# Performance work log

Measured on AMD Instinct MI355X. Metric: run time of the kernel, lower is better.

The kernel has to match this reference:

```python
import jax, jax.numpy as jnp
import numpy as np

N = 50000        # nodes
E = 800000       # random edges (self loops appended inside reference, per PyG default)
IN = 128         # in_channels
H1, C1 = 8, 64   # conv1: heads, hidden_channels
NUM_CLASSES = 2  # conv2 out (heads=1, concat=False)
NEG_SLOPE = 0.2  # PyG GATConv default LeakyReLU slope


def setup_inputs() -> dict:
    key = jax.random.key(0)
    ks = jax.random.split(key, 12)
    x = jax.random.normal(ks[0], (N, IN), dtype=jnp.float32)
    edge_index = jax.random.randint(ks[1], (2, E), 0, N)
    # conv1 params: W1 [IN, H1*C1], att vectors [H1, C1], bias [H1*C1]
    W1 = jax.random.normal(ks[2], (IN, H1 * C1), dtype=jnp.float32) / np.sqrt(IN)
    a_src1 = jax.random.normal(ks[3], (H1, C1), dtype=jnp.float32) / np.sqrt(C1)
    a_dst1 = jax.random.normal(ks[4], (H1, C1), dtype=jnp.float32) / np.sqrt(C1)
    b1 = jnp.zeros((H1 * C1,), dtype=jnp.float32)
    # conv2 params: heads=1, out=NUM_CLASSES
    W2 = jax.random.normal(ks[5], (H1 * C1, 1 * NUM_CLASSES), dtype=jnp.float32) / np.sqrt(H1 * C1)
    a_src2 = jax.random.normal(ks[6], (1, NUM_CLASSES), dtype=jnp.float32) / np.sqrt(NUM_CLASSES)
    a_dst2 = jax.random.normal(ks[7], (1, NUM_CLASSES), dtype=jnp.float32) / np.sqrt(NUM_CLASSES)
    b2 = jnp.zeros((NUM_CLASSES,), dtype=jnp.float32)
    return {"x": x, "edge_index": edge_index, "W1": W1, "a_src1": a_src1,
            "a_dst1": a_dst1, "b1": b1, "W2": W2, "a_src2": a_src2,
            "a_dst2": a_dst2, "b2": b2}


def gat_layer(x, src, dst, W, a_src, a_dst, bias, concat):
    n = x.shape[0]
    heads, ch = a_src.shape
    h = (x @ W).reshape(n, heads, ch)                      # [N,H,C]
    alpha_s = jnp.einsum('nhc,hc->nh', h, a_src)           # per-node src score
    alpha_d = jnp.einsum('nhc,hc->nh', h, a_dst)           # per-node dst score
    e = jax.nn.leaky_relu(alpha_s[src] + alpha_d[dst], NEG_SLOPE)  # [Etot,H]
    # segment softmax over edges grouped by destination node
    m = jax.ops.segment_max(e, dst, num_segments=n)
    ex = jnp.exp(e - m[dst])
    den = jax.ops.segment_sum(ex, dst, num_segments=n)
    alpha = ex / den[dst]                                  # [Etot,H]
    out = jax.ops.segment_sum(h[src] * alpha[:, :, None], dst, num_segments=n)  # [N,H,C]
    out = out.reshape(n, heads * ch) if concat else out.mean(axis=1)
    return out + bias


def reference(x, edge_index, W1, a_src1, a_dst1, b1, W2, a_src2, a_dst2, b2):
    n = x.shape[0]
    loops = jnp.arange(n, dtype=edge_index.dtype)
    src = jnp.concatenate([edge_index[0], loops])   # PyG add_self_loops=True
    dst = jnp.concatenate([edge_index[1], loops])
    h = gat_layer(x, src, dst, W1, a_src1, a_dst1, b1, concat=True)   # [N, H1*C1]
    h = jax.nn.elu(h)
    # dropout is identity in eval mode
    out = gat_layer(h, src, dst, W2, a_src2, a_dst2, b2, concat=False)  # [N, 2]
    return out
```

## Files before the change

kernel.cpp:

```cpp
#include <hip/hip_runtime.h>
#include <hip/hip_bf16.h>

#define NEG 0.2f
#define BKT 64

typedef __attribute__((ext_vector_type(8))) short bf16x8;
typedef __attribute__((ext_vector_type(4))) float f32x4;
typedef __attribute__((ext_vector_type(4))) unsigned int u32x4;

static __device__ __forceinline__ unsigned short f2bf(float f) {
    union { float f; unsigned u; } v; v.f = f;
    unsigned r = v.u + 0x7fff + ((v.u >> 16) & 1);
    return (unsigned short)(r >> 16);
}
static __device__ __forceinline__ float bf_lo(unsigned u) {
    return __uint_as_float(u << 16);
}
static __device__ __forceinline__ float bf_hi(unsigned u) {
    return __uint_as_float(u & 0xffff0000u);
}

__global__ void k_init(int* __restrict__ deg, unsigned short* __restrict__ csr, int n) {
    int v = blockIdx.x * 256 + threadIdx.x;
    if (v >= n) return;
    deg[v] = 1;
    csr[(size_t)v * BKT] = (unsigned short)v;
}

__global__ __launch_bounds__(256) void k_big(const int* __restrict__ ei,
                                             int* __restrict__ deg,
                                             unsigned short* __restrict__ csr,
                                             const float* __restrict__ x,
                                             const float* __restrict__ W1,
                                             const float* __restrict__ a_src,
                                             const float* __restrict__ a_dst,
                                             unsigned short* __restrict__ h1b,
                                             float* __restrict__ as1,
                                             float* __restrict__ ad1,
                                             int E_, int n, int gblocks) {
    int tid = threadIdx.x;
    if ((int)blockIdx.x >= gblocks) {
        int e = (blockIdx.x - gblocks) * 256 + tid;
        if (e >= E_) return;
        int s = ei[e], d = ei[E_ + e];
        int slot = atomicAdd(&deg[d], 1);
        if (slot < BKT) csr[(size_t)d * BKT + slot] = (unsigned short)s;
        return;
    }
    __shared__ unsigned short stg[4][16][72];
    int wave = tid >> 6, lane = tid & 63;
    int l15 = lane & 15, q = lane >> 4;
    int rowblk = blockIdx.x * 256 + wave * 64;

    bf16x8 xf[4][4];
    #pragma unroll
    for (int st = 0; st < 4; st++) {
        int ar = rowblk + st * 16 + l15; if (ar > n - 1) ar = n - 1;
        const float* ap = x + (size_t)ar * 128 + q * 8;
        #pragma unroll
        for (int kb = 0; kb < 4; kb++) {
            float4 v0 = *(const float4*)(ap + kb * 32);
            float4 v1 = *(const float4*)(ap + kb * 32 + 4);
            xf[st][kb][0] = (short)f2bf(v0.x); xf[st][kb][1] = (short)f2bf(v0.y);
            xf[st][kb][2] = (short)f2bf(v0.z); xf[st][kb][3] = (short)f2bf(v0.w);
            xf[st][kb][4] = (short)f2bf(v1.x); xf[st][kb][5] = (short)f2bf(v1.y);
            xf[st][kb][6] = (short)f2bf(v1.z); xf[st][kb][7] = (short)f2bf(v1.w);
        }
    }

    for (int j = 0; j < 8; j++) {
        int col0 = j * 64;
        bf16x8 bfr[4][4];
        #pragma unroll
        for (int kb = 0; kb < 4; kb++)
            #pragma unroll
            for (int t = 0; t < 4; t++) {
                const float* wp = W1 + (size_t)(kb * 32 + q * 8) * 512 + col0 + t * 16 + l15;
                #pragma unroll
                for (int e = 0; e < 8; e++)
                    bfr[kb][t][e] = (short)f2bf(wp[(size_t)e * 512]);
            }
        float asv[4], adv[4];
        #pragma unroll
        for (int t = 0; t < 4; t++) {
            asv[t] = a_src[j * 64 + t * 16 + l15];
            adv[t] = a_dst[j * 64 + t * 16 + l15];
        }

        #pragma unroll
        for (int st = 0; st < 4; st++) {
            int row0 = rowblk + st * 16;
            f32x4 acc[4] = {};
            #pragma unroll
            for (int kb = 0; kb < 4; kb++)
                #pragma unroll
                for (int t = 0; t < 4; t++)
                    acc[t] = __builtin_amdgcn_mfma_f32_16x16x32_bf16(xf[st][kb], bfr[kb][t], acc[t], 0, 0, 0);
            #pragma unroll
            for (int t = 0; t < 4; t++)
                #pragma unroll
                for (int r = 0; r < 4; r++)
                    stg[wave][q * 4 + r][t * 16 + l15] = f2bf(acc[t][r]);
            #pragma unroll
            for (int p = 0; p < 2; p++) {
                int lr = p * 8 + (lane >> 3);
                int row = row0 + lr;
                int cd = (lane & 7) * 8;
                uint4 vv = *(const uint4*)&stg[wave][lr][cd];
                int slice = 2 * j + (cd >> 5);
                if (row < n)
                    *(uint4*)(h1b + ((size_t)slice * n + row) * 32 + (cd & 31)) = vv;
            }
            float ps[4], pd[4];
            #pragma unroll
            for (int r = 0; r < 4; r++) {
                ps[r] = acc[0][r] * asv[0] + acc[1][r] * asv[1]
                      + acc[2][r] * asv[2] + acc[3][r] * asv[3];
                pd[r] = acc[0][r] * adv[0] + acc[1][r] * adv[1]
                      + acc[2][r] * adv[2] + acc[3][r] * adv[3];
                #pragma unroll
                for (int off = 1; off < 16; off <<= 1) {
                    ps[r] += __shfl_xor(ps[r], off, 64);
                    pd[r] += __shfl_xor(pd[r], off, 64);
                }
            }
            if (l15 < 4) {
                int r = l15;
                float vps = ps[0], vpd = pd[0];
                if (r == 1) { vps = ps[1]; vpd = pd[1]; }
                if (r == 2) { vps = ps[2]; vpd = pd[2]; }
                if (r == 3) { vps = ps[3]; vpd = pd[3]; }
                int row = row0 + q * 4 + r;
                if (row < n) {
                    as1[(size_t)j * n + row] = vps;
                    ad1[(size_t)j * n + row] = vpd;
                }
            }
        }
    }
}

#define ACC1(Wt_, Hv_) \
    acc[0] = fmaf(Wt_, bf_lo(Hv_.x), acc[0]); \
    acc[1] = fmaf(Wt_, bf_hi(Hv_.x), acc[1]); \
    acc[2] = fmaf(Wt_, bf_lo(Hv_.y), acc[2]); \
    acc[3] = fmaf(Wt_, bf_hi(Hv_.y), acc[3]); \
    acc[4] = fmaf(Wt_, bf_lo(Hv_.z), acc[4]); \
    acc[5] = fmaf(Wt_, bf_hi(Hv_.z), acc[5]); \
    acc[6] = fmaf(Wt_, bf_lo(Hv_.w), acc[6]); \
    acc[7] = fmaf(Wt_, bf_hi(Hv_.w), acc[7]);

__global__ __launch_bounds__(256) void k_agg1(const unsigned short* __restrict__ h1b,
                                              const float* __restrict__ as1,
                                              const float* __restrict__ ad1,
                                              const float* __restrict__ b1,
                                              const float* __restrict__ W2,
                                              const int* __restrict__ deg,
                                              const unsigned short* __restrict__ csr,
                                              float* __restrict__ part,
                                              int n, int bpp) {
    int b = blockIdx.x;
    int xcd = b & 7;
    int t = b >> 3;
    int sp = (t >= bpp) ? 1 : 0;
    int j = t - sp * bpp;
    int slice = xcd + 8 * sp;
    int head = slice >> 1;

    __shared__ unsigned short idx[4][16][72];

    int tid = threadIdx.x;
    int lane = tid & 63, wave = tid >> 6;
    int g = lane >> 2, sub = lane & 3;
    int v = j * 64 + wave * 16 + g;
    bool act = v < n;
    int vc = act ? v : (n - 1);

    const u32x4* cb = (const u32x4*)(csr + (size_t)vc * BKT);
    u32x4 c0 = __builtin_nontemporal_load(cb + sub);
    u32x4 c1 = __builtin_nontemporal_load(cb + 4 + sub);
    *(u32x4*)&idx[wave][g][sub * 8] = c0;
    *(u32x4*)&idx[wave][g][32 + sub * 8] = c1;
    __syncthreads();

    const unsigned short* hs = h1b + (size_t)slice * n * 32 + sub * 8;
    const float* as1h = as1 + (size_t)head * n;
    const unsigned short* ip = &idx[wave][g][0];

    float adh = 0.f;
    int dv = 0;
    if (act) {
        adh = ad1[(size_t)head * n + v];
        dv = deg[v];
        if (dv > BKT) dv = BKT;
    }

    float s = 0.f;
    float acc[8] = {};
    int i = 0;
    for (; i + 8 <= dv; i += 8) {
        ushort4 ua = *(const ushort4*)(ip + i);
        ushort4 ub = *(const ushort4*)(ip + i + 4);
        int u0 = ua.x, u1 = ua.y, u2 = ua.z, u3 = ua.w;
        int u4 = ub.x, u5 = ub.y, u6 = ub.z, u7 = ub.w;
        float e0 = as1h[u0], e1 = as1h[u1], e2 = as1h[u2], e3 = as1h[u3];
        float e4 = as1h[u4], e5 = as1h[u5], e6 = as1h[u6], e7 = as1h[u7];
        uint4 h0 = *(const uint4*)(hs + (size_t)u0 * 32);
        uint4 h1 = *(const uint4*)(hs + (size_t)u1 * 32);
        uint4 h2 = *(const uint4*)(hs + (size_t)u2 * 32);
        uint4 h3 = *(const uint4*)(hs + (size_t)u3 * 32);
        uint4 h4 = *(const uint4*)(hs + (size_t)u4 * 32);
        uint4 h5 = *(const uint4*)(hs + (size_t)u5 * 32);
        uint4 h6 = *(const uint4*)(hs + (size_t)u6 * 32);
        uint4 h7 = *(const uint4*)(hs + (size_t)u7 * 32);
        e0 += adh; e1 += adh; e2 += adh; e3 += adh;
        e4 += adh; e5 += adh; e6 += adh; e7 += adh;
        e0 = (e0 >= 0.f) ? e0 : NEG * e0;
        e1 = (e1 >= 0.f) ? e1 : NEG * e1;
        e2 = (e2 >= 0.f) ? e2 : NEG * e2;
        e3 = (e3 >= 0.f) ? e3 : NEG * e3;
        e4 = (e4 >= 0.f) ? e4 : NEG * e4;
        e5 = (e5 >= 0.f) ? e5 : NEG * e5;
        e6 = (e6 >= 0.f) ? e6 : NEG * e6;
        e7 = (e7 >= 0.f) ? e7 : NEG * e7;
        float w0 = __expf(e0), w1 = __expf(e1), w2 = __expf(e2), w3 = __expf(e3);
        float w4 = __expf(e4), w5 = __expf(e5), w6 = __expf(e6), w7 = __expf(e7);
        s += ((w0 + w1) + (w2 + w3)) + ((w4 + w5) + (w6 + w7));
        ACC1(w0, h0) ACC1(w1, h1) ACC1(w2, h2) ACC1(w3, h3)
        ACC1(w4, h4) ACC1(w5, h5) ACC1(w6, h6) ACC1(w7, h7)
    }
    for (; i + 4 <= dv; i += 4) {
        ushort4 uu = *(const ushort4*)(ip + i);
        int u0 = uu.x, u1 = uu.y, u2 = uu.z, u3 = uu.w;
        float e0 = as1h[u0], e1 = as1h[u1], e2 = as1h[u2], e3 = as1h[u3];
        uint4 h0 = *(const uint4*)(hs + (size_t)u0 * 32);
        uint4 h1 = *(const uint4*)(hs + (size_t)u1 * 32);
        uint4 h2 = *(const uint4*)(hs + (size_t)u2 * 32);
        uint4 h3 = *(const uint4*)(hs + (size_t)u3 * 32);
        e0 += adh; e1 += adh; e2 += adh; e3 += adh;
        e0 = (e0 >= 0.f) ? e0 : NEG * e0;
        e1 = (e1 >= 0.f) ? e1 : NEG * e1;
        e2 = (e2 >= 0.f) ? e2 : NEG * e2;
        e3 = (e3 >= 0.f) ? e3 : NEG * e3;
        float w0 = __expf(e0), w1 = __expf(e1), w2 = __expf(e2), w3 = __expf(e3);
        s += (w0 + w1) + (w2 + w3);
        ACC1(w0, h0) ACC1(w1, h1) ACC1(w2, h2) ACC1(w3, h3)
    }
    for (; i < dv; i++) {
        int u = ip[i];
        float e = as1h[u] + adh;
        e = (e >= 0.f) ? e : NEG * e;
        float w = __expf(e);
        s += w;
        uint4 hv = *(const uint4*)(hs + (size_t)u * 32);
        ACC1(w, hv)
    }

    float inv = 1.0f / s;
    int cbase = slice * 32 + sub * 8;
    float p0 = 0.f, p1 = 0.f;
    #pragma unroll
    for (int k2 = 0; k2 < 8; k2++) {
        float o = acc[k2] * inv + b1[cbase + k2];
        o = (o > 0.f) ? o : (__expf(o) - 1.0f);
        p0 = fmaf(o, W2[(cbase + k2) * 2], p0);
        p1 = fmaf(o, W2[(cbase + k2) * 2 + 1], p1);
    }
    p0 += __shfl_xor(p0, 1, 64); p0 += __shfl_xor(p0, 2, 64);
    p1 += __shfl_xor(p1, 1, 64); p1 += __shfl_xor(p1, 2, 64);
    if (act && sub == 0) {
        float* pp = part + ((size_t)slice * n + v) * 2;
        __builtin_nontemporal_store(p0, pp);
        __builtin_nontemporal_store(p1, pp + 1);
    }
}

__global__ void k_red(const float* __restrict__ part, float* __restrict__ h2, int n) {
    int v = blockIdx.x * 256 + threadIdx.x;
    if (v >= n) return;
    float s0 = 0.f, s1 = 0.f;
    #pragma unroll
    for (int p = 0; p < 16; p++) {
        float2 pv = *(const float2*)(part + ((size_t)p * n + v) * 2);
        s0 += pv.x; s1 += pv.y;
    }
    h2[2 * v] = s0;
    h2[2 * v + 1] = s1;
}

__global__ __launch_bounds__(256) void k_agg2(const float* __restrict__ h2,
                                              const float* __restrict__ a_src2,
                                              const float* __restrict__ a_dst2,
                                              const float* __restrict__ b2,
                                              const int* __restrict__ deg,
                                              const unsigned short* __restrict__ csr,
                                              float* __restrict__ out, int n) {
    int tid = threadIdx.x;
    int lane = tid & 63, wave = tid >> 6;
    int sub = lane & 7, g = lane >> 3;
    int v = blockIdx.x * 32 + wave * 8 + g;
    if (v >= n) return;
    int dv = deg[v]; if (dv > BKT) dv = BKT;
    const unsigned short* cp = csr + (size_t)v * BKT;
    float sa0 = a_src2[0], sa1 = a_src2[1];
    float da0 = a_dst2[0], da1 = a_dst2[1];
    float2 hv = *(const float2*)(h2 + 2 * v);
    float adv = hv.x * da0 + hv.y * da1;
    float s = 0.f, a0 = 0.f, a1 = 0.f;
    for (int i = sub; i < dv; i += 8) {
        int u = cp[i];
        float2 hu = *(const float2*)(h2 + 2 * u);
        float e = hu.x * sa0 + hu.y * sa1 + adv;
        e = (e >= 0.f) ? e : NEG * e;
        float w = __expf(e);
        s += w;
        a0 = fmaf(w, hu.x, a0);
        a1 = fmaf(w, hu.y, a1);
    }
    #pragma unroll
    for (int off = 1; off < 8; off <<= 1) {
        s  += __shfl_xor(s, off, 64);
        a0 += __shfl_xor(a0, off, 64);
        a1 += __shfl_xor(a1, off, 64);
    }
    if (sub == 0) {
        float inv = 1.0f / s;
        out[2 * v]     = a0 * inv + b2[0];
        out[2 * v + 1] = a1 * inv + b2[1];
    }
}

extern "C" void kernel_launch(void* const* d_in, const int* in_sizes, int n_in,
                              void* d_out, int out_size, void* d_ws, size_t ws_size,
                              hipStream_t stream) {
    const float* x      = (const float*)d_in[0];
    const int*   ei     = (const int*)d_in[1];
    const float* W1     = (const float*)d_in[2];
    const float* a_src1 = (const float*)d_in[3];
    const float* a_dst1 = (const float*)d_in[4];
    const float* b1     = (const float*)d_in[5];
    const float* W2     = (const float*)d_in[6];
    const float* a_src2 = (const float*)d_in[7];
    const float* a_dst2 = (const float*)d_in[8];
    const float* b2     = (const float*)d_in[9];
    float* out = (float*)d_out;

    int n  = in_sizes[0] / 128;
    int E_ = in_sizes[1] / 2;
    int rblk = (n + 255) / 256;

    char* w = (char*)d_ws;
    auto alloc = [&](size_t bytes) {
        char* p = w; w += (bytes + 255) & ~(size_t)255; return p;
    };
    int*            deg    = (int*)alloc((size_t)n * 4);
    unsigned short* csr    = (unsigned short*)alloc((size_t)n * BKT * 2);
    unsigned short* h1b    = (unsigned short*)alloc((size_t)n * 16 * 32 * 2);
    float*          as1    = (float*)alloc((size_t)n * 8 * 4);
    float*          ad1    = (float*)alloc((size_t)n * 8 * 4);
    float*          part   = (float*)alloc((size_t)n * 16 * 2 * 4);
    float*          h2     = (float*)alloc((size_t)n * 2 * 4);

    int nb256 = (n + 255) / 256;
    k_init<<<nb256, 256, 0, stream>>>(deg, csr, n);

    int gblocks = rblk;
    int sblocks = (E_ + 255) / 256;
    k_big<<<gblocks + sblocks, 256, 0, stream>>>(ei, deg, csr, x, W1,
                                                 a_src1, a_dst1, h1b, as1, ad1,
                                                 E_, n, gblocks);

    int bpp = (n + 63) / 64;
    k_agg1<<<16 * bpp, 256, 0, stream>>>(h1b, as1, ad1, b1, W2, deg, csr,
                                         part, n, bpp);

    k_red<<<nb256, 256, 0, stream>>>(part, h2, n);

    int ab = (n + 31) / 32;
    k_agg2<<<ab, 256, 0, stream>>>(h2, a_src2, a_dst2, b2, deg, csr, out, n);
}
```

Baseline: 297.7 us.

## Precompute per-edge attention weights once in bf16 before layer-1 aggregation

```diff
diff --git a/kernel.cpp b/kernel.cpp
--- a/kernel.cpp
+++ b/kernel.cpp
@@ -18,6 +18,9 @@
 }
 static __device__ __forceinline__ float bf_hi(unsigned u) {
     return __uint_as_float(u & 0xffff0000u);
+}
+static __device__ __forceinline__ float bfu(unsigned short u) {
+    return __uint_as_float(((unsigned)u) << 16);
 }
 
 __global__ void k_init(int* __restrict__ deg, unsigned short* __restrict__ csr, int n) {
@@ -132,11 +135,52 @@
                 if (r == 3) { vps = ps[3]; vpd = pd[3]; }
                 int row = row0 + q * 4 + r;
                 if (row < n) {
-                    as1[(size_t)j * n + row] = vps;
-                    ad1[(size_t)j * n + row] = vpd;
+                    as1[(size_t)row * 8 + j] = vps;
+                    ad1[(size_t)row * 8 + j] = vpd;
                 }
             }
         }
+    }
+}
+
+__global__ __launch_bounds__(256) void k_wt(const float* __restrict__ as1,
+                                            const float* __restrict__ ad1,
+                                            const int* __restrict__ deg,
+                                            const unsigned short* __restrict__ csr,
+                                            unsigned short* __restrict__ W,
+                                            int n) {
+    int tid = threadIdx.x;
+    int lane = tid & 63, wave = tid >> 6;
+    int g8 = lane >> 3, h = lane & 7;
+    int v = blockIdx.x * 32 + wave * 8 + g8;
+    if (v >= n) return;
+    int dv = deg[v]; if (dv > BKT) dv = BKT;
+    float adv = ad1[(size_t)v * 8 + h];
+    const unsigned short* cp = csr + (size_t)v * BKT;
+    unsigned short* wp = W + ((size_t)v * 8 + h) * 64;
+    int i = 0;
+    for (; i + 4 <= dv; i += 4) {
+        ushort4 uu = *(const ushort4*)(cp + i);
+        float e0 = as1[(size_t)uu.x * 8 + h] + adv;
+        float e1 = as1[(size_t)uu.y * 8 + h] + adv;
+        float e2 = as1[(size_t)uu.z * 8 + h] + adv;
+        float e3 = as1[(size_t)uu.w * 8 + h] + adv;
+        e0 = (e0 >= 0.f) ? e0 : NEG * e0;
+        e1 = (e1 >= 0.f) ? e1 : NEG * e1;
+        e2 = (e2 >= 0.f) ? e2 : NEG * e2;
+        e3 = (e3 >= 0.f) ? e3 : NEG * e3;
+        ushort4 o;
+        o.x = f2bf(__expf(e0));
+        o.y = f2bf(__expf(e1));
+        o.z = f2bf(__expf(e2));
+        o.w = f2bf(__expf(e3));
+        *(ushort4*)(wp + i) = o;
+    }
+    for (; i < dv; i++) {
+        int u = cp[i];
+        float e = as1[(size_t)u * 8 + h] + adv;
+        e = (e >= 0.f) ? e : NEG * e;
+        wp[i] = f2bf(__expf(e));
     }
 }
 
@@ -151,8 +195,7 @@
     acc[7] = fmaf(Wt_, bf_hi(Hv_.w), acc[7]);
 
 __global__ __launch_bounds__(256) void k_agg1(const unsigned short* __restrict__ h1b,
-                                              const float* __restrict__ as1,
-                                              const float* __restrict__ ad1,
+                                              const unsigned short* __restrict__ Wt,
                                               const float* __restrict__ b1,
                                               const float* __restrict__ W2,
                                               const int* __restrict__ deg,
@@ -168,6 +211,7 @@
     int head = slice >> 1;
 
     __shared__ unsigned short idx[4][16][72];
+    __shared__ unsigned short wls[4][16][72];
 
     int tid = threadIdx.x;
     int lane = tid & 63, wave = tid >> 6;
@@ -179,18 +223,21 @@
     const u32x4* cb = (const u32x4*)(csr + (size_t)vc * BKT);
     u32x4 c0 = __builtin_nontemporal_load(cb + sub);
     u32x4 c1 = __builtin_nontemporal_load(cb + 4 + sub);
+    const u32x4* wb = (const u32x4*)(Wt + ((size_t)vc * 8 + head) * 64);
+    u32x4 w0_ = __builtin_nontemporal_load(wb + sub);
+    u32x4 w1_ = __builtin_nontemporal_load(wb + 4 + sub);
     *(u32x4*)&idx[wave][g][sub * 8] = c0;
     *(u32x4*)&idx[wave][g][32 + sub * 8] = c1;
+    *(u32x4*)&wls[wave][g][sub * 8] = w0_;
+    *(u32x4*)&wls[wave][g][32 + sub * 8] = w1_;
     __syncthreads();
 
     const unsigned short* hs = h1b + (size_t)slice * n * 32 + sub * 8;
-    const float* as1h = as1 + (size_t)head * n;
     const unsigned short* ip = &idx[wave][g][0];
-
-    float adh = 0.f;
+    const unsigned short* wq = &wls[wave][g][0];
+
     int dv = 0;
     if (act) {
-        adh = ad1[(size_t)head * n + v];
         dv = deg[v];
         if (dv > BKT) dv = BKT;
     }
@@ -201,10 +248,10 @@
     for (; i + 8 <= dv; i += 8) {
         ushort4 ua = *(const ushort4*)(ip + i);
         ushort4 ub = *(const ushort4*)(ip + i + 4);
+        ushort4 wa = *(const ushort4*)(wq + i);
+        ushort4 wc = *(const ushort4*)(wq + i + 4);
         int u0 = ua.x, u1 = ua.y, u2 = ua.z, u3 = ua.w;
         int u4 = ub.x, u5 = ub.y, u6 = ub.z, u7 = ub.w;
-        float e0 = as1h[u0], e1 = as1h[u1], e2 = as1h[u2], e3 = as1h[u3];
-        float e4 = as1h[u4], e5 = as1h[u5], e6 = as1h[u6], e7 = as1h[u7];
         uint4 h0 = *(const uint4*)(hs + (size_t)u0 * 32);
         uint4 h1 = *(const uint4*)(hs + (size_t)u1 * 32);
         uint4 h2 = *(const uint4*)(hs + (size_t)u2 * 32);
@@ -213,44 +260,27 @@
         uint4 h5 = *(const uint4*)(hs + (size_t)u5 * 32);
         uint4 h6 = *(const uint4*)(hs + (size_t)u6 * 32);
         uint4 h7 = *(const uint4*)(hs + (size_t)u7 * 32);
-        e0 += adh; e1 += adh; e2 += adh; e3 += adh;
-        e4 += adh; e5 += adh; e6 += adh; e7 += adh;
-        e0 = (e0 >= 0.f) ? e0 : NEG * e0;
-        e1 = (e1 >= 0.f) ? e1 : NEG * e1;
-        e2 = (e2 >= 0.f) ? e2 : NEG * e2;
-        e3 = (e3 >= 0.f) ? e3 : NEG * e3;
-        e4 = (e4 >= 0.f) ? e4 : NEG * e4;
-        e5 = (e5 >= 0.f) ? e5 : NEG * e5;
-        e6 = (e6 >= 0.f) ? e6 : NEG * e6;
-        e7 = (e7 >= 0.f) ? e7 : NEG * e7;
-        float w0 = __expf(e0), w1 = __expf(e1), w2 = __expf(e2), w3 = __expf(e3);
-        float w4 = __expf(e4), w5 = __expf(e5), w6 = __expf(e6), w7 = __expf(e7);
+        float w0 = bfu(wa.x), w1 = bfu(wa.y), w2 = bfu(wa.z), w3 = bfu(wa.w);
+        float w4 = bfu(wc.x), w5 = bfu(wc.y), w6 = bfu(wc.z), w7 = bfu(wc.w);
         s += ((w0 + w1) + (w2 + w3)) + ((w4 + w5) + (w6 + w7));
         ACC1(w0, h0) ACC1(w1, h1) ACC1(w2, h2) ACC1(w3, h3)
         ACC1(w4, h4) ACC1(w5, h5) ACC1(w6, h6) ACC1(w7, h7)
     }
     for (; i + 4 <= dv; i += 4) {
         ushort4 uu = *(const ushort4*)(ip + i);
+        ushort4 wa = *(const ushort4*)(wq + i);
         int u0 = uu.x, u1 = uu.y, u2 = uu.z, u3 = uu.w;
-        float e0 = as1h[u0], e1 = as1h[u1], e2 = as1h[u2], e3 = as1h[u3];
         uint4 h0 = *(const uint4*)(hs + (size_t)u0 * 32);
         uint4 h1 = *(const uint4*)(hs + (size_t)u1 * 32);
         uint4 h2 = *(const uint4*)(hs + (size_t)u2 * 32);
         uint4 h3 = *(const uint4*)(hs + (size_t)u3 * 32);
-        e0 += adh; e1 += adh; e2 += adh; e3 += adh;
-        e0 = (e0 >= 0.f) ? e0 : NEG * e0;
-        e1 = (e1 >= 0.f) ? e1 : NEG * e1;
-        e2 = (e2 >= 0.f) ? e2 : NEG * e2;
-        e3 = (e3 >= 0.f) ? e3 : NEG * e3;
-        float w0 = __expf(e0), w1 = __expf(e1), w2 = __expf(e2), w3 = __expf(e3);
+        float w0 = bfu(wa.x), w1 = bfu(wa.y), w2 = bfu(wa.z), w3 = bfu(wa.w);
         s += (w0 + w1) + (w2 + w3);
         ACC1(w0, h0) ACC1(w1, h1) ACC1(w2, h2) ACC1(w3, h3)
     }
     for (; i < dv; i++) {
         int u = ip[i];
-        float e = as1h[u] + adh;
-        e = (e >= 0.f) ? e : NEG * e;
-        float w = __expf(e);
+        float w = bfu(wq[i]);
         s += w;
         uint4 hv = *(const uint4*)(hs + (size_t)u * 32);
         ACC1(w, hv)
@@ -358,6 +388,7 @@
     unsigned short* h1b    = (unsigned short*)alloc((size_t)n * 16 * 32 * 2);
     float*          as1    = (float*)alloc((size_t)n * 8 * 4);
     float*          ad1    = (float*)alloc((size_t)n * 8 * 4);
+    unsigned short* Wt     = (unsigned short*)alloc((size_t)n * 8 * 64 * 2);
     float*          part   = (float*)alloc((size_t)n * 16 * 2 * 4);
     float*          h2     = (float*)alloc((size_t)n * 2 * 4);
 
@@ -370,8 +401,11 @@
                                                  a_src1, a_dst1, h1b, as1, ad1,
                                                  E_, n, gblocks);
 
+    int wtb = (n + 31) / 32;
+    k_wt<<<wtb, 256, 0, stream>>>(as1, ad1, deg, csr, Wt, n);
+
     int bpp = (n + 63) / 64;
-    k_agg1<<<16 * bpp, 256, 0, stream>>>(h1b, as1, ad1, b1, W2, deg, csr,
+    k_agg1<<<16 * bpp, 256, 0, stream>>>(h1b, Wt, b1, W2, deg, csr,
                                          part, n, bpp);
 
     k_red<<<nb256, 256, 0, stream>>>(part, h2, n);
```

New measurement: 322.6 us. 1.08x slower.
